# Performance work log

Measured on AMD Instinct MI355X. Metric: run time of the kernel, lower is better.

The kernel has to match this reference:

```python
import jax, jax.numpy as jnp
import numpy as np

D_MODEL = 1024
N_HEADS = 16
D_K = D_MODEL // N_HEADS


def rotate_half(x):
    x1, x2 = x[..., : x.shape[-1] // 2], x[..., x.shape[-1] // 2:]
    return jnp.concatenate((-x2, x1), axis=-1)


def rope_cos_sin(seq_len, d_k, dtype):
    inv_freq = 1.0 / (10000.0 ** (jnp.arange(0, d_k, 2, dtype=jnp.float32) / d_k))
    t = jnp.arange(seq_len, dtype=jnp.float32)
    freqs = jnp.outer(t, inv_freq)            # [S, d_k/2]
    emb = jnp.concatenate((freqs, freqs), -1) # [S, d_k]
    return jnp.cos(emb).astype(dtype), jnp.sin(emb).astype(dtype)


def setup_inputs() -> dict:
    key = jax.random.key(0)
    ks = jax.random.split(key, 8)
    B, S = 1, 2048
    q = jax.random.normal(ks[0], (B, S, D_MODEL), jnp.float32)
    k = jax.random.normal(ks[1], (B, S, D_MODEL), jnp.float32)
    v = jax.random.normal(ks[2], (B, S, D_MODEL), jnp.float32)
    # xavier-uniform-ish weights for [d_model, d_model]
    bound = float(np.sqrt(6.0 / (D_MODEL + D_MODEL)))
    def W(kk):
        return jax.random.uniform(kk, (D_MODEL, D_MODEL), jnp.float32, -bound, bound)
    return {
        "query": q, "key": k, "value": v,
        "w_q": W(ks[3]), "w_k": W(ks[4]), "w_v": W(ks[5]),
        "w_o": W(ks[6]), "b_o": jnp.zeros((D_MODEL,), jnp.float32),
    }


def reference(query, key, value, w_q, w_k, w_v, w_o, b_o):
    B, Sq, _ = query.shape
    Sk = key.shape[1]
    # projections (torch Linear: x @ W.T)
    Q = (query @ w_q.T).reshape(B, Sq, N_HEADS, D_K).transpose(0, 2, 1, 3)
    K = (key @ w_k.T).reshape(B, Sk, N_HEADS, D_K).transpose(0, 2, 1, 3)
    V = (value @ w_v.T).reshape(B, Sk, N_HEADS, D_K).transpose(0, 2, 1, 3)
    # RoPE on Q and K (over head dim d_k)
    cos_q, sin_q = rope_cos_sin(Sq, D_K, Q.dtype)
    cos_k, sin_k = (cos_q, sin_q) if Sk == Sq else rope_cos_sin(Sk, D_K, K.dtype)
    Q = Q * cos_q + rotate_half(Q) * sin_q
    K = K * cos_k + rotate_half(K) * sin_k
    scores = jnp.einsum("bhqd,bhkd->bhqk", Q, K) / jnp.sqrt(jnp.float32(D_K)).astype(Q.dtype)
    attn = jax.nn.softmax(scores, axis=-1)          # [B,H,Sq,Sk]
    ctx = jnp.einsum("bhqk,bhkd->bhqd", attn, V)    # [B,H,Sq,d_k]
    ctx = ctx.transpose(0, 2, 1, 3).reshape(B, Sq, D_MODEL)
    out = ctx @ w_o.T + b_o
    return out, attn
```

## Files before the change

### kernel.cpp

```cpp
#include <hip/hip_runtime.h>
#include <hip/hip_bf16.h>

using short8 = __attribute__((ext_vector_type(8))) short;
using f32x4  = __attribute__((ext_vector_type(4))) float;

#define SEQ   2048
#define DM    1024
#define NHEAD 16
#define MB    1048576

static __device__ __forceinline__ short f2bf(float f) {
    union { __hip_bfloat16 b; short s; } u;
    u.b = __float2bfloat16(f);
    return u.s;
}
static __device__ __forceinline__ f32x4 mfma_bf16(short8 a, short8 b, f32x4 c) {
    return __builtin_amdgcn_mfma_f32_16x16x32_bf16(a, b, c, 0, 0, 0);
}

__global__ __launch_bounds__(256) void prep_kernel(
    const float* __restrict__ q, const float* __restrict__ k, const float* __restrict__ v,
    const float* __restrict__ wq, const float* __restrict__ wk, const float* __restrict__ wv,
    const float* __restrict__ wo, short* __restrict__ bf,
    float* __restrict__ cosT, float* __restrict__ sinT)
{
    long t = (long)blockIdx.x * 256 + threadIdx.x;
    if (t < 1310720) {
        long e0 = t * 8;
        const float* src; long off;
        if      (e0 < 2L*MB) { src = q;  off = e0; }
        else if (e0 < 4L*MB) { src = k;  off = e0 - 2L*MB; }
        else if (e0 < 6L*MB) { src = v;  off = e0 - 4L*MB; }
        else if (e0 < 7L*MB) { src = wq; off = e0 - 6L*MB; }
        else if (e0 < 8L*MB) { src = wk; off = e0 - 7L*MB; }
        else if (e0 < 9L*MB) { src = wv; off = e0 - 8L*MB; }
        else                 { src = wo; off = e0 - 9L*MB; }
        float4 a = *(const float4*)(src + off);
        float4 b = *(const float4*)(src + off + 4);
        short8 o;
        o[0]=f2bf(a.x); o[1]=f2bf(a.y); o[2]=f2bf(a.z); o[3]=f2bf(a.w);
        o[4]=f2bf(b.x); o[5]=f2bf(b.y); o[6]=f2bf(b.z); o[7]=f2bf(b.w);
        *(short8*)(bf + e0) = o;
    } else {
        long tt = t - 1310720;
        int s = (int)(tt >> 5), j = (int)(tt & 31);
        float invf = __expf(-(float)j * (9.210340371976184f / 32.0f));
        float arg = (float)s * invf;
        cosT[tt] = cosf(arg);
        sinT[tt] = sinf(arg);
    }
}

__global__ __launch_bounds__(256, 2) void gemm_qkv(
    short* __restrict__ wsbf, const float* __restrict__ cosT,
    const float* __restrict__ sinT)
{
    __shared__ short As[128 * 64];
    __shared__ short Bs[128 * 64];
    const int tid  = threadIdx.x;
    const int lane = tid & 63;
    const int wave = tid >> 6;
    const int q4   = lane >> 4;
    const int l16  = lane & 15;
    const int wm   = wave >> 1;
    const int wn   = wave & 1;
    const int m0   = blockIdx.y * 128;
    const int n0   = blockIdx.x * 128;
    const int z    = blockIdx.z;

    const short* A = wsbf + (size_t)z * (2*MB);
    const short* W = wsbf + 6*(size_t)MB + (size_t)z * MB;

    f32x4 zero = {0.f, 0.f, 0.f, 0.f};
    f32x4 acc[4][4];
    #pragma unroll
    for (int i = 0; i < 4; ++i)
        #pragma unroll
        for (int j = 0; j < 4; ++j) acc[i][j] = zero;

    for (int k0 = 0; k0 < 1024; k0 += 64) {
        __syncthreads();
        #pragma unroll
        for (int r = 0; r < 4; ++r) {
            int g = r * 256 + tid;
            int row = g >> 3, c8 = g & 7;
            int sw = c8 ^ (row & 7);
            *(short8*)&As[row*64 + sw*8] = *(const short8*)(A + (size_t)(m0+row)*1024 + k0 + c8*8);
            *(short8*)&Bs[row*64 + sw*8] = *(const short8*)(W + (size_t)(n0+row)*1024 + k0 + c8*8);
        }
        __syncthreads();
        #pragma unroll
        for (int kk = 0; kk < 2; ++kk) {
            short8 af[4], bfr[4];
            #pragma unroll
            for (int i = 0; i < 4; ++i) {
                int ra = wm*64 + i*16 + l16;
                af[i]  = *(const short8*)&As[ra*64 + (((kk*4+q4) ^ (ra&7))*8)];
                int rb = wn*64 + i*16 + l16;
                bfr[i] = *(const short8*)&Bs[rb*64 + (((kk*4+q4) ^ (rb&7))*8)];
            }
            #pragma unroll
            for (int i = 0; i < 4; ++i)
                #pragma unroll
                for (int j = 0; j < 4; ++j)
                    acc[i][j] = mfma_bf16(af[i], bfr[j], acc[i][j]);
        }
    }

    const int h = (n0 >> 6) + wn;
    if (z < 2) {
        short* dst = wsbf + (size_t)(10 + 2*z) * MB;
        #pragma unroll
        for (int i = 0; i < 4; ++i) {
            #pragma unroll
            for (int jj = 0; jj < 4; ++jj) {
                int s = m0 + wm*64 + i*16 + q4*4 + jj;
                float c0 = cosT[(s<<5) + l16],      s0 = sinT[(s<<5) + l16];
                float c1 = cosT[(s<<5) + 16 + l16], s1 = sinT[(s<<5) + 16 + l16];
                float v0 = acc[i][0][jj], v1 = acc[i][1][jj];
                float v2 = acc[i][2][jj], v3 = acc[i][3][jj];
                size_t base = ((size_t)h*SEQ + s)*64;
                dst[base + l16]      = f2bf(v0*c0 - v2*s0);
                dst[base + 16 + l16] = f2bf(v1*c1 - v3*s1);
                dst[base + 32 + l16] = f2bf(v2*c0 + v0*s0);
                dst[base + 48 + l16] = f2bf(v3*c1 + v1*s1);
            }
        }
    } else {
        short* dst = wsbf + (size_t)14 * MB;
        #pragma unroll
        for (int i = 0; i < 4; ++i)
            #pragma unroll
            for (int j = 0; j < 4; ++j)
                #pragma unroll
                for (int jj = 0; jj < 4; ++jj) {
                    int s = m0 + wm*64 + i*16 + q4*4 + jj;
                    int d = j*16 + l16;
                    dst[((size_t)h*64 + d)*SEQ + s] = f2bf(acc[i][j][jj]);
                }
    }
}

__global__ __launch_bounds__(256, 2) void attn_kernel(
    const short* __restrict__ wsbf, short* __restrict__ ctxout,
    float* __restrict__ attn)
{
    __shared__ short Qs[64 * 64];
    __shared__ short Ks[128 * 64];
    __shared__ short Vs[64 * 128];
    __shared__ short Ps[4][16 * 128];
    const int tid = threadIdx.x, lane = tid & 63, wave = tid >> 6;
    const int q4 = lane >> 4, l16 = lane & 15;
    const int h = blockIdx.y, qt0 = blockIdx.x * 64;
    const short* Qg = wsbf + (size_t)10*MB + ((size_t)h*SEQ + qt0)*64;
    const short* Kg = wsbf + (size_t)12*MB + (size_t)h*SEQ*64;
    const short* Vg = wsbf + (size_t)14*MB + (size_t)h*64*SEQ;

    #pragma unroll
    for (int r = 0; r < 2; ++r) {
        int g = r*256 + tid; int row = g >> 3, c8 = g & 7;
        *(short8*)&Qs[row*64 + ((c8 ^ (row&7))*8)] = *(const short8*)(Qg + (size_t)row*64 + c8*8);
    }
    __syncthreads();
    const int ra = wave*16 + l16;
    short8 a_q[2];
    #pragma unroll
    for (int kk = 0; kk < 2; ++kk)
        a_q[kk] = *(const short8*)&Qs[ra*64 + (((kk*4+q4) ^ (ra&7))*8)];

    f32x4 zero = {0.f, 0.f, 0.f, 0.f};
    f32x4 ctx[4] = {zero, zero, zero, zero};
    float rs[4] = {0.f, 0.f, 0.f, 0.f};
    const int frw = ((l16 & 7) + 2*(l16 >> 3)) & 7;

    for (int kt = 0; kt < 16; ++kt) {
        __syncthreads();
        #pragma unroll
        for (int r = 0; r < 4; ++r) {
            int g = r*256 + tid; int row = g >> 3, c8 = g & 7;
            *(short8*)&Ks[row*64 + ((c8 ^ (row&7))*8)] =
                *(const short8*)(Kg + (size_t)(kt*128 + row)*64 + c8*8);
        }
        #pragma unroll
        for (int r = 0; r < 4; ++r) {
            int g = r*256 + tid; int row = g >> 4, c16 = g & 15;
            *(short8*)&Vs[row*128 + ((c16 ^ (row&7))*8)] =
                *(const short8*)(Vg + (size_t)row*SEQ + kt*128 + c16*8);
        }
        __syncthreads();
        #pragma unroll
        for (int nt = 0; nt < 8; ++nt) {
            f32x4 acc = zero;
            #pragma unroll
            for (int kk = 0; kk < 2; ++kk) {
                int rb = nt*16 + l16;
                short8 b = *(const short8*)&Ks[rb*64 + (((kk*4+q4) ^ (rb&7))*8)];
                acc = mfma_bf16(a_q[kk], b, acc);
            }
            #pragma unroll
            for (int jj = 0; jj < 4; ++jj) {
                float p = __expf(acc[jj] * 0.125f);
                rs[jj] += p;
                int prow = q4*4 + jj;
                int col  = nt*16 + l16;
                int fr   = ((prow & 7) + 2*(prow >> 3)) & 7;
                int phys = (col >> 3) ^ fr;
                Ps[wave][prow*128 + phys*8 + (col & 7)] = f2bf(p);
            }
        }
        #pragma unroll
        for (int kks = 0; kks < 4; ++kks) {
            short8 a = *(const short8*)&Ps[wave][l16*128 + (((kks*4+q4) ^ frw)*8)];
            #pragma unroll
            for (int dt = 0; dt < 4; ++dt) {
                int rv = dt*16 + l16;
                short8 b = *(const short8*)&Vs[rv*128 + (((kks*4+q4) ^ (rv&7))*8)];
                ctx[dt] = mfma_bf16(a, b, ctx[dt]);
            }
        }
    }

    #pragma unroll
    for (int jj = 0; jj < 4; ++jj)
        #pragma unroll
        for (int m = 1; m < 16; m <<= 1)
            rs[jj] += __shfl_xor(rs[jj], m);
    float irs[4];
    #pragma unroll
    for (int jj = 0; jj < 4; ++jj) irs[jj] = 1.0f / rs[jj];

    const int qbase = qt0 + wave*16 + q4*4;
    #pragma unroll
    for (int dt = 0; dt < 4; ++dt)
        #pragma unroll
        for (int jj = 0; jj < 4; ++jj)
            ctxout[(size_t)(qbase + jj)*1024 + h*64 + dt*16 + l16] = f2bf(ctx[dt][jj] * irs[jj]);

    float* arow = attn + (size_t)h*SEQ*SEQ;
    for (int kt = 0; kt < 16; ++kt) {
        __syncthreads();
        #pragma unroll
        for (int r = 0; r < 4; ++r) {
            int g = r*256 + tid; int row = g >> 3, c8 = g & 7;
            *(short8*)&Ks[row*64 + ((c8 ^ (row&7))*8)] =
                *(const short8*)(Kg + (size_t)(kt*128 + row)*64 + c8*8);
        }
        __syncthreads();
        #pragma unroll
        for (int nt = 0; nt < 8; ++nt) {
            f32x4 acc = zero;
            #pragma unroll
            for (int kk = 0; kk < 2; ++kk) {
                int rb = nt*16 + l16;
                short8 b = *(const short8*)&Ks[rb*64 + (((kk*4+q4) ^ (rb&7))*8)];
                acc = mfma_bf16(a_q[kk], b, acc);
            }
            #pragma unroll
            for (int jj = 0; jj < 4; ++jj)
                arow[(size_t)(qbase + jj)*SEQ + kt*128 + nt*16 + l16] =
                    __expf(acc[jj] * 0.125f) * irs[jj];
        }
    }
}

__global__ __launch_bounds__(256, 2) void gemm_out(
    const short* __restrict__ wsbf, const float* __restrict__ bo,
    float* __restrict__ out)
{
    __shared__ short As[128 * 64];
    __shared__ short Bs[64 * 64];
    const int tid = threadIdx.x, lane = tid & 63, wave = tid >> 6;
    const int q4 = lane >> 4, l16 = lane & 15;
    const int m0 = blockIdx.y * 128, n0 = blockIdx.x * 64;
    const short* A = wsbf + 16*(size_t)MB;
    const short* W = wsbf + 9*(size_t)MB;

    f32x4 zero = {0.f, 0.f, 0.f, 0.f};
    f32x4 acc[2][4];
    #pragma unroll
    for (int i = 0; i < 2; ++i)
        #pragma unroll
        for (int j = 0; j < 4; ++j) acc[i][j] = zero;

    for (int k0 = 0; k0 < 1024; k0 += 64) {
        __syncthreads();
        #pragma unroll
        for (int r = 0; r < 4; ++r) {
            int g = r * 256 + tid;
            int row = g >> 3, c8 = g & 7;
            *(short8*)&As[row*64 + ((c8 ^ (row&7))*8)] =
                *(const short8*)(A + (size_t)(m0+row)*1024 + k0 + c8*8);
        }
        #pragma unroll
        for (int r = 0; r < 2; ++r) {
            int g = r * 256 + tid;
            int row = g >> 3, c8 = g & 7;
            *(short8*)&Bs[row*64 + ((c8 ^ (row&7))*8)] =
                *(const short8*)(W + (size_t)(n0+row)*1024 + k0 + c8*8);
        }
        __syncthreads();
        #pragma unroll
        for (int kk = 0; kk < 2; ++kk) {
            short8 af[2], bfr[4];
            #pragma unroll
            for (int i = 0; i < 2; ++i) {
                int ra = wave*32 + i*16 + l16;
                af[i] = *(const short8*)&As[ra*64 + (((kk*4+q4) ^ (ra&7))*8)];
            }
            #pragma unroll
            for (int j = 0; j < 4; ++j) {
                int rb = j*16 + l16;
                bfr[j] = *(const short8*)&Bs[rb*64 + (((kk*4+q4) ^ (rb&7))*8)];
            }
            #pragma unroll
            for (int i = 0; i < 2; ++i)
                #pragma unroll
                for (int j = 0; j < 4; ++j)
                    acc[i][j] = mfma_bf16(af[i], bfr[j], acc[i][j]);
        }
    }

    #pragma unroll
    for (int i = 0; i < 2; ++i)
        #pragma unroll
        for (int j = 0; j < 4; ++j)
            #pragma unroll
            for (int jj = 0; jj < 4; ++jj) {
                int gr = m0 + wave*32 + i*16 + q4*4 + jj;
                int gc = n0 + j*16 + l16;
                out[(size_t)gr*1024 + gc] = acc[i][j][jj] + bo[gc];
            }
}

extern "C" void kernel_launch(void* const* d_in, const int* in_sizes, int n_in,
                              void* d_out, int out_size, void* d_ws, size_t ws_size,
                              hipStream_t stream)
{
    const float* q  = (const float*)d_in[0];
    const float* k  = (const float*)d_in[1];
    const float* v  = (const float*)d_in[2];
    const float* wq = (const float*)d_in[3];
    const float* wk = (const float*)d_in[4];
    const float* wv = (const float*)d_in[5];
    const float* wo = (const float*)d_in[6];
    const float* bo = (const float*)d_in[7];

    short* wsbf = (short*)d_ws;
    float* cosT = (float*)((char*)d_ws + (size_t)36*MB);
    float* sinT = cosT + 65536;
    float* out  = (float*)d_out;
    float* attn = out + (size_t)SEQ*DM;

    hipLaunchKernelGGL(prep_kernel, dim3(5376), dim3(256), 0, stream,
                       q, k, v, wq, wk, wv, wo, wsbf, cosT, sinT);
    hipLaunchKernelGGL(gemm_qkv, dim3(8, 16, 3), dim3(256), 0, stream,
                       wsbf, cosT, sinT);
    hipLaunchKernelGGL(attn_kernel, dim3(32, 16), dim3(256), 0, stream,
                       wsbf, wsbf + (size_t)16*MB, attn);
    hipLaunchKernelGGL(gemm_out, dim3(16, 16), dim3(256), 0, stream,
                       wsbf, bo, out);
}
```

Measured before the change: 402.9 us.

## Use direct global-to-LDS loads and double-buffer K tiles in attention

```diff
diff --git a/kernel.cpp b/kernel.cpp
--- a/kernel.cpp
+++ b/kernel.cpp
@@ -8,6 +8,10 @@
 #define DM    1024
 #define NHEAD 16
 #define MB    1048576
+
+#define GLD16(GP, LP) __builtin_amdgcn_global_load_lds(                      \
+    (const __attribute__((address_space(1))) void*)(GP),                     \
+    (__attribute__((address_space(3))) void*)(LP), 16, 0, 0)
 
 static __device__ __forceinline__ short f2bf(float f) {
     union { __hip_bfloat16 b; short s; } u;
@@ -78,15 +82,16 @@
         #pragma unroll
         for (int j = 0; j < 4; ++j) acc[i][j] = zero;
 
+    const int r8 = tid >> 3, c8 = tid & 7;
+
     for (int k0 = 0; k0 < 1024; k0 += 64) {
         __syncthreads();
         #pragma unroll
         for (int r = 0; r < 4; ++r) {
-            int g = r * 256 + tid;
-            int row = g >> 3, c8 = g & 7;
-            int sw = c8 ^ (row & 7);
-            *(short8*)&As[row*64 + sw*8] = *(const short8*)(A + (size_t)(m0+row)*1024 + k0 + c8*8);
-            *(short8*)&Bs[row*64 + sw*8] = *(const short8*)(W + (size_t)(n0+row)*1024 + k0 + c8*8);
+            int row = r*32 + r8;
+            int sw  = c8 ^ (row & 7);
+            GLD16(A + (size_t)(m0+row)*1024 + k0 + sw*8, &As[(r*256 + tid)*8]);
+            GLD16(W + (size_t)(n0+row)*1024 + k0 + sw*8, &Bs[(r*256 + tid)*8]);
         }
         __syncthreads();
         #pragma unroll
@@ -146,7 +151,7 @@
     float* __restrict__ attn)
 {
     __shared__ short Qs[64 * 64];
-    __shared__ short Ks[128 * 64];
+    __shared__ short Ks[2][128 * 64];
     __shared__ short Vs[64 * 128];
     __shared__ short Ps[4][16 * 128];
     const int tid = threadIdx.x, lane = tid & 63, wave = tid >> 6;
@@ -156,12 +161,35 @@
     const short* Kg = wsbf + (size_t)12*MB + (size_t)h*SEQ*64;
     const short* Vg = wsbf + (size_t)14*MB + (size_t)h*64*SEQ;
 
+    const int r8  = tid >> 3, c8  = tid & 7;
+    const int r16 = tid >> 4, c16 = tid & 15;
+
+    auto stageK = [&](int kt, short* buf) {
+        #pragma unroll
+        for (int r = 0; r < 4; ++r) {
+            int row = r*32 + r8;
+            int sw  = c8 ^ (row & 7);
+            GLD16(Kg + (size_t)(kt*128 + row)*64 + sw*8, buf + (r*256 + tid)*8);
+        }
+    };
+    auto stageV = [&](int kt) {
+        #pragma unroll
+        for (int r = 0; r < 4; ++r) {
+            int row = r*16 + r16;
+            int sw  = c16 ^ (row & 7);
+            GLD16(Vg + (size_t)row*SEQ + kt*128 + sw*8, &Vs[(r*256 + tid)*8]);
+        }
+    };
+
     #pragma unroll
     for (int r = 0; r < 2; ++r) {
-        int g = r*256 + tid; int row = g >> 3, c8 = g & 7;
-        *(short8*)&Qs[row*64 + ((c8 ^ (row&7))*8)] = *(const short8*)(Qg + (size_t)row*64 + c8*8);
-    }
+        int row = r*32 + r8;
+        int sw  = c8 ^ (row & 7);
+        GLD16(Qg + (size_t)row*64 + sw*8, &Qs[(r*256 + tid)*8]);
+    }
+    stageK(0, Ks[0]);
     __syncthreads();
+
     const int ra = wave*16 + l16;
     short8 a_q[2];
     #pragma unroll
@@ -174,27 +202,17 @@
     const int frw = ((l16 & 7) + 2*(l16 >> 3)) & 7;
 
     for (int kt = 0; kt < 16; ++kt) {
-        __syncthreads();
-        #pragma unroll
-        for (int r = 0; r < 4; ++r) {
-            int g = r*256 + tid; int row = g >> 3, c8 = g & 7;
-            *(short8*)&Ks[row*64 + ((c8 ^ (row&7))*8)] =
-                *(const short8*)(Kg + (size_t)(kt*128 + row)*64 + c8*8);
-        }
-        #pragma unroll
-        for (int r = 0; r < 4; ++r) {
-            int g = r*256 + tid; int row = g >> 4, c16 = g & 15;
-            *(short8*)&Vs[row*128 + ((c16 ^ (row&7))*8)] =
-                *(const short8*)(Vg + (size_t)row*SEQ + kt*128 + c16*8);
-        }
-        __syncthreads();
+        const short* Kb = (kt & 1) ? Ks[1] : Ks[0];
+        short*       Kn = (kt & 1) ? Ks[0] : Ks[1];
+        stageV(kt);
+        if (kt < 15) stageK(kt + 1, Kn);
         #pragma unroll
         for (int nt = 0; nt < 8; ++nt) {
             f32x4 acc = zero;
             #pragma unroll
             for (int kk = 0; kk < 2; ++kk) {
                 int rb = nt*16 + l16;
-                short8 b = *(const short8*)&Ks[rb*64 + (((kk*4+q4) ^ (rb&7))*8)];
+                short8 b = *(const short8*)&Kb[rb*64 + (((kk*4+q4) ^ (rb&7))*8)];
                 acc = mfma_bf16(a_q[kk], b, acc);
             }
             #pragma unroll
@@ -208,6 +226,9 @@
                 Ps[wave][prow*128 + phys*8 + (col & 7)] = f2bf(p);
             }
         }
+        if (kt < 15) asm volatile("s_waitcnt vmcnt(4) lgkmcnt(0)" ::: "memory");
+        else         asm volatile("s_waitcnt vmcnt(0) lgkmcnt(0)" ::: "memory");
+        __builtin_amdgcn_s_barrier();
         #pragma unroll
         for (int kks = 0; kks < 4; ++kks) {
             short8 a = *(const short8*)&Ps[wave][l16*128 + (((kks*4+q4) ^ frw)*8)];
@@ -218,6 +239,8 @@
                 ctx[dt] = mfma_bf16(a, b, ctx[dt]);
             }
         }
+        asm volatile("s_waitcnt vmcnt(0) lgkmcnt(0)" ::: "memory");
+        __builtin_amdgcn_s_barrier();
     }
 
     #pragma unroll
@@ -236,23 +259,22 @@
         for (int jj = 0; jj < 4; ++jj)
             ctxout[(size_t)(qbase + jj)*1024 + h*64 + dt*16 + l16] = f2bf(ctx[dt][jj] * irs[jj]);
 
+    stageK(0, Ks[0]);
+    asm volatile("s_waitcnt vmcnt(0) lgkmcnt(0)" ::: "memory");
+    __builtin_amdgcn_s_barrier();
+
     float* arow = attn + (size_t)h*SEQ*SEQ;
     for (int kt = 0; kt < 16; ++kt) {
-        __syncthreads();
-        #pragma unroll
-        for (int r = 0; r < 4; ++r) {
-            int g = r*256 + tid; int row = g >> 3, c8 = g & 7;
-            *(short8*)&Ks[row*64 + ((c8 ^ (row&7))*8)] =
-                *(const short8*)(Kg + (size_t)(kt*128 + row)*64 + c8*8);
-        }
-        __syncthreads();
+        const short* Kb = (kt & 1) ? Ks[1] : Ks[0];
+        short*       Kn = (kt & 1) ? Ks[0] : Ks[1];
+        if (kt < 15) stageK(kt + 1, Kn);
         #pragma unroll
         for (int nt = 0; nt < 8; ++nt) {
             f32x4 acc = zero;
             #pragma unroll
             for (int kk = 0; kk < 2; ++kk) {
                 int rb = nt*16 + l16;
-                short8 b = *(const short8*)&Ks[rb*64 + (((kk*4+q4) ^ (rb&7))*8)];
+                short8 b = *(const short8*)&Kb[rb*64 + (((kk*4+q4) ^ (rb&7))*8)];
                 acc = mfma_bf16(a_q[kk], b, acc);
             }
             #pragma unroll
@@ -260,6 +282,8 @@
                 arow[(size_t)(qbase + jj)*SEQ + kt*128 + nt*16 + l16] =
                     __expf(acc[jj] * 0.125f) * irs[jj];
         }
+        asm volatile("s_waitcnt vmcnt(32) lgkmcnt(0)" ::: "memory");
+        __builtin_amdgcn_s_barrier();
     }
 }
 
@@ -282,21 +306,21 @@
         #pragma unroll
         for (int j = 0; j < 4; ++j) acc[i][j] = zero;
 
+    const int r8 = tid >> 3, c8 = tid & 7;
+
     for (int k0 = 0; k0 < 1024; k0 += 64) {
         __syncthreads();
         #pragma unroll
         for (int r = 0; r < 4; ++r) {
-            int g = r * 256 + tid;
-            int row = g >> 3, c8 = g & 7;
-            *(short8*)&As[row*64 + ((c8 ^ (row&7))*8)] =
-                *(const short8*)(A + (size_t)(m0+row)*1024 + k0 + c8*8);
+            int row = r*32 + r8;
+            int sw  = c8 ^ (row & 7);
+            GLD16(A + (size_t)(m0+row)*1024 + k0 + sw*8, &As[(r*256 + tid)*8]);
         }
         #pragma unroll
         for (int r = 0; r < 2; ++r) {
-            int g = r * 256 + tid;
-            int row = g >> 3, c8 = g & 7;
-            *(short8*)&Bs[row*64 + ((c8 ^ (row&7))*8)] =
-                *(const short8*)(W + (size_t)(n0+row)*1024 + k0 + c8*8);
+            int row = r*32 + r8;
+            int sw  = c8 ^ (row & 7);
+            GLD16(W + (size_t)(n0+row)*1024 + k0 + sw*8, &Bs[(r*256 + tid)*8]);
         }
         __syncthreads();
         #pragma unroll
```

Result: no change. 410.4 us (+1.9%).
